# Kernel tuning notes

Hardware: AMD Instinct MI355X
Metric: run time of the kernel (lower is better)

Reference implementation:

```python
import jax, jax.numpy as jnp
import numpy as np

B, N, FIN = 4, 4096, 128
H, U = 4, 32

def setup_inputs() -> dict:
    key = jax.random.key(0)
    k = jax.random.split(key, 6)
    x = jax.random.normal(k[0], (B, N, FIN), dtype=jnp.float32)
    adj = (jax.random.uniform(k[1], (B, N, N)) < 0.05).astype(jnp.float32)
    glorot = lambda kk, shape, fi, fo: jax.random.uniform(kk, shape, jnp.float32,
                                                          -np.sqrt(6.0/(fi+fo)), np.sqrt(6.0/(fi+fo)))
    W = glorot(k[2], (FIN, H*U), FIN, H*U)
    a_src = glorot(k[3], (H, U, 1), U, 1)
    a_dst = glorot(k[4], (H, U, 1), U, 1)
    bias = jnp.zeros((H*U,), dtype=jnp.float32)
    return {"x": x, "adj": adj, "W": W, "a_src": a_src, "a_dst": a_dst, "bias": bias}

def reference(x, adj, W, a_src, a_dst, bias):
    # inference mode: attention dropout is a no-op
    b, n, _ = x.shape
    h_heads, u = a_src.shape[0], a_src.shape[1]
    # add self-loops, clip to {0,1}
    adj = jnp.clip(adj + jnp.eye(n, dtype=adj.dtype)[None], 0.0, 1.0)
    h = (x @ W).reshape(b, n, h_heads, u).transpose(0, 2, 1, 3)      # [B,H,N,U]
    f1 = jnp.einsum('bhnu,hu->bhn', h, a_src[..., 0])                # [B,H,N]
    f2 = jnp.einsum('bhnu,hu->bhn', h, a_dst[..., 0])                # [B,H,N]
    e = f1[:, :, :, None] + f2[:, :, None, :]                        # [B,H,N,N]
    e = jnp.where(e > 0, e, 0.2 * e)                                 # LeakyReLU(0.2)
    e = jnp.where(adj[:, None] > 0.0, e, jnp.float32(-1e9))
    alpha = jax.nn.softmax(e, axis=-1)
    out = jnp.einsum('bhij,bhju->bhiu', alpha, h)                    # [B,H,N,U]
    out = out.transpose(0, 2, 1, 3).reshape(b, n, h_heads * u) + bias
    return jnp.where(out > 0, out, jnp.expm1(out))                   # ELU
```

## Files before the change

kernel.cpp:

```cpp
#include <hip/hip_runtime.h>
#include <math.h>

#define NB   4
#define NN   4096
#define FIN  128
#define FOUT 128
#define NH   4
#define UU   32

#define K1_ROWS 64
#define K1_RT   8
#define K1_CT   4
#define XPAD    132

__global__ __launch_bounds__(256) void k1_feat(
    const float* __restrict__ x, const float* __restrict__ W,
    const float* __restrict__ a_src, const float* __restrict__ a_dst,
    float* __restrict__ hfeat, float* __restrict__ f1g, float* __restrict__ f2g)
{
    __shared__ __align__(16) float Wq[32 * FOUT];
    __shared__ __align__(16) float xs[K1_ROWS * XPAD];

    const int tid  = threadIdx.x;
    const int row0 = blockIdx.x * K1_ROWS;

    const float4* x4 = (const float4*)(x + (size_t)row0 * FIN);
    for (int idx = tid; idx < K1_ROWS * FIN / 4; idx += 256) {
        int r = idx >> 5, q = idx & 31;
        *(float4*)(xs + r * XPAD + q * 4) = x4[idx];
    }

    const int cg = tid & 31;
    const int rg = tid >> 5;
    float acc[K1_RT][K1_CT];
    #pragma unroll
    for (int rr = 0; rr < K1_RT; rr++)
        #pragma unroll
        for (int cc = 0; cc < K1_CT; cc++) acc[rr][cc] = 0.f;

    for (int kt = 0; kt < 4; kt++) {
        __syncthreads();
        for (int idx = tid; idx < 32 * FOUT / 4; idx += 256)
            ((float4*)Wq)[idx] = ((const float4*)W)[kt * 1024 + idx];
        __syncthreads();
        #pragma unroll
        for (int k4 = 0; k4 < 8; k4++) {
            const int kb = kt * 32 + k4 * 4;
            float4 xv[K1_RT];
            #pragma unroll
            for (int rr = 0; rr < K1_RT; rr++)
                xv[rr] = *(const float4*)(xs + (rg * K1_RT + rr) * XPAD + kb);
            #pragma unroll
            for (int kk = 0; kk < 4; kk++) {
                float wv[K1_CT];
                #pragma unroll
                for (int cc = 0; cc < K1_CT; cc++)
                    wv[cc] = Wq[(k4 * 4 + kk) * FOUT + cg + 32 * cc];
                #pragma unroll
                for (int rr = 0; rr < K1_RT; rr++) {
                    float xk = ((const float*)&xv[rr])[kk];
                    #pragma unroll
                    for (int cc = 0; cc < K1_CT; cc++)
                        acc[rr][cc] = fmaf(xk, wv[cc], acc[rr][cc]);
                }
            }
        }
    }
    __syncthreads();
    #pragma unroll
    for (int rr = 0; rr < K1_RT; rr++)
        #pragma unroll
        for (int cc = 0; cc < K1_CT; cc++)
            xs[(rg * K1_RT + rr) * XPAD + cg + 32 * cc] = acc[rr][cc];
    __syncthreads();

    float4* h4 = (float4*)(hfeat + (size_t)row0 * FOUT);
    for (int idx = tid; idx < K1_ROWS * FOUT / 4; idx += 256) {
        int r = idx >> 5, q = idx & 31;
        h4[idx] = *(const float4*)(xs + r * XPAD + q * 4);
    }

    for (int task = tid; task < K1_ROWS * NH * 2; task += 256) {
        int row = task >> 3;
        int head = (task >> 1) & 3;
        int which = task & 1;
        const float* av = which ? a_dst : a_src;
        float s = 0.f;
        #pragma unroll
        for (int u = 0; u < UU; u++)
            s += xs[row * XPAD + head * UU + u] * av[head * UU + u];
        float* dst = which ? f2g : f1g;
        dst[(size_t)(row0 + row) * NH + head] = s;
    }
}

#define CAP  512
#define APAD 516
#define PPAD 132

__global__ __launch_bounds__(256) void k2_gat(
    const float* __restrict__ adj, const float* __restrict__ hfeat,
    const float* __restrict__ f1g, const float* __restrict__ f2g,
    const float* __restrict__ bias, float* __restrict__ out)
{
    const int row  = blockIdx.x;
    const int b    = row >> 12;
    const int i    = row & (NN - 1);
    const int tid  = threadIdx.x;
    const int lane = tid & 63;
    const int wv   = tid >> 6;

    __shared__ int   nbr[CAP];
    __shared__ float alpha[NH][APAD];
    __shared__ float part[8][PPAD];
    __shared__ float inv_s[NH];
    __shared__ int   cnt_s;

    if (tid == 0) cnt_s = 0;
    __syncthreads();

    const float4* arow = (const float4*)(adj + (size_t)row * NN);
    float4 v[4];
    #pragma unroll
    for (int it = 0; it < 4; it++)
        v[it] = arow[wv * 256 + it * 64 + lane];

    const unsigned long long below = (1ull << lane) - 1ull;
    #pragma unroll
    for (int it = 0; it < 4; it++) {
        const int jb = (wv * 256 + it * 64 + lane) << 2;
        const bool p0 = (v[it].x > 0.f) | (jb + 0 == i);
        const bool p1 = (v[it].y > 0.f) | (jb + 1 == i);
        const bool p2 = (v[it].z > 0.f) | (jb + 2 == i);
        const bool p3 = (v[it].w > 0.f) | (jb + 3 == i);
        unsigned long long m0 = __ballot(p0), m1 = __ballot(p1);
        unsigned long long m2 = __ballot(p2), m3 = __ballot(p3);
        int c0 = __popcll(m0), c1 = __popcll(m1), c2 = __popcll(m2), c3 = __popcll(m3);
        int base = 0;
        if (lane == 0) base = atomicAdd(&cnt_s, c0 + c1 + c2 + c3);
        base = __shfl(base, 0, 64);
        if (p0) { int p = base + __popcll(m0 & below);                if (p < CAP) nbr[p] = jb + 0; }
        if (p1) { int p = base + c0 + __popcll(m1 & below);           if (p < CAP) nbr[p] = jb + 1; }
        if (p2) { int p = base + c0 + c1 + __popcll(m2 & below);      if (p < CAP) nbr[p] = jb + 2; }
        if (p3) { int p = base + c0 + c1 + c2 + __popcll(m3 & below); if (p < CAP) nbr[p] = jb + 3; }
    }
    __syncthreads();
    const int K = (cnt_s < CAP) ? cnt_s : CAP;

    const float4 f1v = ((const float4*)f1g)[row];
    for (int k = tid; k < K; k += 256) {
        int j = nbr[k];
        float4 f2v = ((const float4*)f2g)[(size_t)b * NN + j];
        float e0 = f1v.x + f2v.x; e0 = e0 > 0.f ? e0 : 0.2f * e0;
        float e1 = f1v.y + f2v.y; e1 = e1 > 0.f ? e1 : 0.2f * e1;
        float e2 = f1v.z + f2v.z; e2 = e2 > 0.f ? e2 : 0.2f * e2;
        float e3 = f1v.w + f2v.w; e3 = e3 > 0.f ? e3 : 0.2f * e3;
        alpha[0][k] = e0; alpha[1][k] = e1; alpha[2][k] = e2; alpha[3][k] = e3;
    }
    __syncthreads();

    {
        float m = -1e30f;
        for (int k = lane; k < K; k += 64) m = fmaxf(m, alpha[wv][k]);
        #pragma unroll
        for (int off = 32; off > 0; off >>= 1) m = fmaxf(m, __shfl_xor(m, off, 64));
        float s = 0.f;
        for (int k = lane; k < K; k += 64) {
            float a = __expf(alpha[wv][k] - m);
            alpha[wv][k] = a;
            s += a;
        }
        #pragma unroll
        for (int off = 32; off > 0; off >>= 1) s += __shfl_xor(s, off, 64);
        if (lane == 0) inv_s[wv] = 1.f / s;
    }
    __syncthreads();

    const int cq = tid & 31;
    const int kg = tid >> 5;
    const int hh = cq >> 3;
    const float* hb = hfeat + (size_t)b * NN * FOUT + cq * 4;
    float4 acc = make_float4(0.f, 0.f, 0.f, 0.f);
    int k = kg;
    for (; k + 8 < K; k += 16) {
        int j0 = nbr[k], j1 = nbr[k + 8];
        float a0 = alpha[hh][k], a1 = alpha[hh][k + 8];
        float4 h0 = *(const float4*)(hb + (size_t)j0 * FOUT);
        float4 h1 = *(const float4*)(hb + (size_t)j1 * FOUT);
        acc.x = fmaf(a0, h0.x, acc.x); acc.y = fmaf(a0, h0.y, acc.y);
        acc.z = fmaf(a0, h0.z, acc.z); acc.w = fmaf(a0, h0.w, acc.w);
        acc.x = fmaf(a1, h1.x, acc.x); acc.y = fmaf(a1, h1.y, acc.y);
        acc.z = fmaf(a1, h1.z, acc.z); acc.w = fmaf(a1, h1.w, acc.w);
    }
    if (k < K) {
        int j0 = nbr[k];
        float a0 = alpha[hh][k];
        float4 h0 = *(const float4*)(hb + (size_t)j0 * FOUT);
        acc.x = fmaf(a0, h0.x, acc.x); acc.y = fmaf(a0, h0.y, acc.y);
        acc.z = fmaf(a0, h0.z, acc.z); acc.w = fmaf(a0, h0.w, acc.w);
    }
    *(float4*)&part[kg][cq * 4] = acc;
    __syncthreads();

    if (tid < FOUT) {
        float o = 0.f;
        #pragma unroll
        for (int g = 0; g < 8; g++) o += part[g][tid];
        o = o * inv_s[tid >> 5] + bias[tid];
        o = o > 0.f ? o : expm1f(o);
        out[(size_t)row * FOUT + tid] = o;
    }
}

extern "C" void kernel_launch(void* const* d_in, const int* in_sizes, int n_in,
                              void* d_out, int out_size, void* d_ws, size_t ws_size,
                              hipStream_t stream) {
    const float* x     = (const float*)d_in[0];
    const float* adj   = (const float*)d_in[1];
    const float* W     = (const float*)d_in[2];
    const float* a_src = (const float*)d_in[3];
    const float* a_dst = (const float*)d_in[4];
    const float* bias  = (const float*)d_in[5];
    float* out = (float*)d_out;

    char* ws = (char*)d_ws;
    float* hfeat = (float*)ws;
    float* f1g   = (float*)(ws + (size_t)NB * NN * FOUT * 4);
    float* f2g   = f1g + (size_t)NB * NN * NH;

    k1_feat<<<NB * NN / K1_ROWS, 256, 0, stream>>>(x, W, a_src, a_dst, hfeat, f1g, f2g);
    k2_gat<<<NB * NN, 256, 0, stream>>>(adj, hfeat, f1g, f2g, bias, out);
}
```

Before: 420.7 us.

## Store features in bf16, fuse logit computation into compaction, remap blocks per XCD

Kernel 1 writes projected features as bf16, halving the bytes gathered per neighbor in the aggregation kernel. The neighbor compaction now uses a two-pass per-wave count and prefix instead of a shared atomic, and computes the LeakyReLU logits inline while writing neighbor indices. Block indices are remapped so each XCD processes a single batch, improving L2 reuse of the gathered features. This trades fp32 precision of h for bandwidth and adds a duplicate ballot pass over the adjacency row.

```diff
diff --git a/kernel.cpp b/kernel.cpp
--- a/kernel.cpp
+++ b/kernel.cpp
@@ -8,6 +8,12 @@
 #define NH   4
 #define UU   32
 
+__device__ __forceinline__ unsigned short f2bf(float f) {
+    unsigned u = __float_as_uint(f);
+    u += 0x7fff + ((u >> 16) & 1);
+    return (unsigned short)(u >> 16);
+}
+
 #define K1_ROWS 64
 #define K1_RT   8
 #define K1_CT   4
@@ -16,7 +22,7 @@
 __global__ __launch_bounds__(256) void k1_feat(
     const float* __restrict__ x, const float* __restrict__ W,
     const float* __restrict__ a_src, const float* __restrict__ a_dst,
-    float* __restrict__ hfeat, float* __restrict__ f1g, float* __restrict__ f2g)
+    unsigned short* __restrict__ hbf, float* __restrict__ f1g, float* __restrict__ f2g)
 {
     __shared__ __align__(16) float Wq[32 * FOUT];
     __shared__ __align__(16) float xs[K1_ROWS * XPAD];
@@ -74,10 +80,16 @@
             xs[(rg * K1_RT + rr) * XPAD + cg + 32 * cc] = acc[rr][cc];
     __syncthreads();
 
-    float4* h4 = (float4*)(hfeat + (size_t)row0 * FOUT);
-    for (int idx = tid; idx < K1_ROWS * FOUT / 4; idx += 256) {
-        int r = idx >> 5, q = idx & 31;
-        h4[idx] = *(const float4*)(xs + r * XPAD + q * 4);
+    unsigned short* hrow = hbf + (size_t)row0 * FOUT;
+    for (int idx = tid; idx < K1_ROWS * FOUT / 8; idx += 256) {
+        int r = idx >> 4, q = idx & 15;
+        const float* src = xs + r * XPAD + q * 8;
+        uint4 o;
+        o.x = (unsigned)f2bf(src[0]) | ((unsigned)f2bf(src[1]) << 16);
+        o.y = (unsigned)f2bf(src[2]) | ((unsigned)f2bf(src[3]) << 16);
+        o.z = (unsigned)f2bf(src[4]) | ((unsigned)f2bf(src[5]) << 16);
+        o.w = (unsigned)f2bf(src[6]) | ((unsigned)f2bf(src[7]) << 16);
+        *(uint4*)(hrow + (size_t)r * FOUT + q * 8) = o;
     }
 
     for (int task = tid; task < K1_ROWS * NH * 2; task += 256) {
@@ -94,30 +106,31 @@
     }
 }
 
-#define CAP  512
-#define APAD 516
-#define PPAD 132
+#define CAP   512
+#define APAD  516
+#define PPART 132
+
+__device__ __forceinline__ float lrelu(float e) { return e > 0.f ? e : 0.2f * e; }
 
 __global__ __launch_bounds__(256) void k2_gat(
-    const float* __restrict__ adj, const float* __restrict__ hfeat,
+    const float* __restrict__ adj, const unsigned short* __restrict__ hbf,
     const float* __restrict__ f1g, const float* __restrict__ f2g,
     const float* __restrict__ bias, float* __restrict__ out)
 {
-    const int row  = blockIdx.x;
-    const int b    = row >> 12;
-    const int i    = row & (NN - 1);
+    const int q    = blockIdx.x;
+    const int xcd  = q & 7;
+    const int b    = xcd >> 1;
+    const int i    = ((q >> 3) << 1) | (xcd & 1);
+    const int row  = b * NN + i;
     const int tid  = threadIdx.x;
     const int lane = tid & 63;
     const int wv   = tid >> 6;
 
     __shared__ int   nbr[CAP];
     __shared__ float alpha[NH][APAD];
-    __shared__ float part[8][PPAD];
+    __shared__ float part[16][PPART];
     __shared__ float inv_s[NH];
-    __shared__ int   cnt_s;
-
-    if (tid == 0) cnt_s = 0;
-    __syncthreads();
+    __shared__ int   wcnt[4];
 
     const float4* arow = (const float4*)(adj + (size_t)row * NN);
     float4 v[4];
@@ -126,6 +139,25 @@
         v[it] = arow[wv * 256 + it * 64 + lane];
 
     const unsigned long long below = (1ull << lane) - 1ull;
+    int my_cnt = 0;
+    #pragma unroll
+    for (int it = 0; it < 4; it++) {
+        const int jb = (wv * 256 + it * 64 + lane) << 2;
+        my_cnt += __popcll(__ballot((v[it].x > 0.f) | (jb + 0 == i)));
+        my_cnt += __popcll(__ballot((v[it].y > 0.f) | (jb + 1 == i)));
+        my_cnt += __popcll(__ballot((v[it].z > 0.f) | (jb + 2 == i)));
+        my_cnt += __popcll(__ballot((v[it].w > 0.f) | (jb + 3 == i)));
+    }
+    if (lane == 0) wcnt[wv] = my_cnt;
+    __syncthreads();
+
+    const int w0 = wcnt[0], w1 = wcnt[1], w2 = wcnt[2], w3 = wcnt[3];
+    int run = (wv > 0 ? w0 : 0) + (wv > 1 ? w1 : 0) + (wv > 2 ? w2 : 0);
+    const int total = w0 + w1 + w2 + w3;
+    const int K = (total < CAP) ? total : CAP;
+
+    const float4* f2b = (const float4*)(f2g + (size_t)b * NN * NH);
+    const float4  f1v = ((const float4*)f1g)[row];
     #pragma unroll
     for (int it = 0; it < 4; it++) {
         const int jb = (wv * 256 + it * 64 + lane) << 2;
@@ -136,26 +168,25 @@
         unsigned long long m0 = __ballot(p0), m1 = __ballot(p1);
         unsigned long long m2 = __ballot(p2), m3 = __ballot(p3);
         int c0 = __popcll(m0), c1 = __popcll(m1), c2 = __popcll(m2), c3 = __popcll(m3);
-        int base = 0;
-        if (lane == 0) base = atomicAdd(&cnt_s, c0 + c1 + c2 + c3);
-        base = __shfl(base, 0, 64);
-        if (p0) { int p = base + __popcll(m0 & below);                if (p < CAP) nbr[p] = jb + 0; }
-        if (p1) { int p = base + c0 + __popcll(m1 & below);           if (p < CAP) nbr[p] = jb + 1; }
-        if (p2) { int p = base + c0 + c1 + __popcll(m2 & below);      if (p < CAP) nbr[p] = jb + 2; }
-        if (p3) { int p = base + c0 + c1 + c2 + __popcll(m3 & below); if (p < CAP) nbr[p] = jb + 3; }
-    }
-    __syncthreads();
-    const int K = (cnt_s < CAP) ? cnt_s : CAP;
-
-    const float4 f1v = ((const float4*)f1g)[row];
-    for (int k = tid; k < K; k += 256) {
-        int j = nbr[k];
-        float4 f2v = ((const float4*)f2g)[(size_t)b * NN + j];
-        float e0 = f1v.x + f2v.x; e0 = e0 > 0.f ? e0 : 0.2f * e0;
-        float e1 = f1v.y + f2v.y; e1 = e1 > 0.f ? e1 : 0.2f * e1;
-        float e2 = f1v.z + f2v.z; e2 = e2 > 0.f ? e2 : 0.2f * e2;
-        float e3 = f1v.w + f2v.w; e3 = e3 > 0.f ? e3 : 0.2f * e3;
-        alpha[0][k] = e0; alpha[1][k] = e1; alpha[2][k] = e2; alpha[3][k] = e3;
+        #pragma unroll
+        for (int e = 0; e < 4; e++) {
+            bool pe = e == 0 ? p0 : e == 1 ? p1 : e == 2 ? p2 : p3;
+            unsigned long long me = e == 0 ? m0 : e == 1 ? m1 : e == 2 ? m2 : m3;
+            int pre = e == 0 ? 0 : e == 1 ? c0 : e == 2 ? c0 + c1 : c0 + c1 + c2;
+            if (pe) {
+                int p = run + pre + __popcll(me & below);
+                if (p < CAP) {
+                    int j = jb + e;
+                    nbr[p] = j;
+                    float4 f2v = f2b[j];
+                    alpha[0][p] = lrelu(f1v.x + f2v.x);
+                    alpha[1][p] = lrelu(f1v.y + f2v.y);
+                    alpha[2][p] = lrelu(f1v.z + f2v.z);
+                    alpha[3][p] = lrelu(f1v.w + f2v.w);
+                }
+            }
+        }
+        run += c0 + c1 + c2 + c3;
     }
     __syncthreads();
 
@@ -176,36 +207,52 @@
     }
     __syncthreads();
 
-    const int cq = tid & 31;
-    const int kg = tid >> 5;
-    const int hh = cq >> 3;
-    const float* hb = hfeat + (size_t)b * NN * FOUT + cq * 4;
-    float4 acc = make_float4(0.f, 0.f, 0.f, 0.f);
+    const int cq = tid & 15;
+    const int kg = tid >> 4;
+    const int hh = cq >> 2;
+    const unsigned short* hb = hbf + (size_t)b * NN * FOUT + cq * 8;
+    float acc[8];
+    #pragma unroll
+    for (int t = 0; t < 8; t++) acc[t] = 0.f;
+
     int k = kg;
-    for (; k + 8 < K; k += 16) {
-        int j0 = nbr[k], j1 = nbr[k + 8];
-        float a0 = alpha[hh][k], a1 = alpha[hh][k + 8];
-        float4 h0 = *(const float4*)(hb + (size_t)j0 * FOUT);
-        float4 h1 = *(const float4*)(hb + (size_t)j1 * FOUT);
-        acc.x = fmaf(a0, h0.x, acc.x); acc.y = fmaf(a0, h0.y, acc.y);
-        acc.z = fmaf(a0, h0.z, acc.z); acc.w = fmaf(a0, h0.w, acc.w);
-        acc.x = fmaf(a1, h1.x, acc.x); acc.y = fmaf(a1, h1.y, acc.y);
-        acc.z = fmaf(a1, h1.z, acc.z); acc.w = fmaf(a1, h1.w, acc.w);
+    for (; k + 16 < K; k += 32) {
+        int j0 = nbr[k], j1 = nbr[k + 16];
+        float a0 = alpha[hh][k], a1 = alpha[hh][k + 16];
+        uint4 u4a = *(const uint4*)(hb + (size_t)j0 * FOUT);
+        uint4 u4b = *(const uint4*)(hb + (size_t)j1 * FOUT);
+        const unsigned* u0 = (const unsigned*)&u4a;
+        const unsigned* u1 = (const unsigned*)&u4b;
+        #pragma unroll
+        for (int t = 0; t < 4; t++) {
+            acc[2*t]   = fmaf(a0, __uint_as_float(u0[t] << 16),          acc[2*t]);
+            acc[2*t+1] = fmaf(a0, __uint_as_float(u0[t] & 0xffff0000u),  acc[2*t+1]);
+        }
+        #pragma unroll
+        for (int t = 0; t < 4; t++) {
+            acc[2*t]   = fmaf(a1, __uint_as_float(u1[t] << 16),          acc[2*t]);
+            acc[2*t+1] = fmaf(a1, __uint_as_float(u1[t] & 0xffff0000u),  acc[2*t+1]);
+        }
     }
     if (k < K) {
         int j0 = nbr[k];
         float a0 = alpha[hh][k];
-        float4 h0 = *(const float4*)(hb + (size_t)j0 * FOUT);
-        acc.x = fmaf(a0, h0.x, acc.x); acc.y = fmaf(a0, h0.y, acc.y);
-        acc.z = fmaf(a0, h0.z, acc.z); acc.w = fmaf(a0, h0.w, acc.w);
-    }
-    *(float4*)&part[kg][cq * 4] = acc;
+        uint4 u4a = *(const uint4*)(hb + (size_t)j0 * FOUT);
+        const unsigned* u0 = (const unsigned*)&u4a;
+        #pragma unroll
+        for (int t = 0; t < 4; t++) {
+            acc[2*t]   = fmaf(a0, __uint_as_float(u0[t] << 16),          acc[2*t]);
+            acc[2*t+1] = fmaf(a0, __uint_as_float(u0[t] & 0xffff0000u),  acc[2*t+1]);
+        }
+    }
+    *(float4*)&part[kg][cq * 8]     = *(float4*)&acc[0];
+    *(float4*)&part[kg][cq * 8 + 4] = *(float4*)&acc[4];
     __syncthreads();
 
     if (tid < FOUT) {
         float o = 0.f;
         #pragma unroll
-        for (int g = 0; g < 8; g++) o += part[g][tid];
+        for (int g = 0; g < 16; g++) o += part[g][tid];
         o = o * inv_s[tid >> 5] + bias[tid];
         o = o > 0.f ? o : expm1f(o);
         out[(size_t)row * FOUT + tid] = o;
@@ -224,10 +271,10 @@
     float* out = (float*)d_out;
 
     char* ws = (char*)d_ws;
-    float* hfeat = (float*)ws;
-    float* f1g   = (float*)(ws + (size_t)NB * NN * FOUT * 4);
-    float* f2g   = f1g + (size_t)NB * NN * NH;
-
-    k1_feat<<<NB * NN / K1_ROWS, 256, 0, stream>>>(x, W, a_src, a_dst, hfeat, f1g, f2g);
-    k2_gat<<<NB * NN, 256, 0, stream>>>(adj, hfeat, f1g, f2g, bias, out);
-}
+    unsigned short* hbf = (unsigned short*)ws;
+    float* f1g = (float*)(ws + (size_t)NB * NN * FOUT * 2);
+    float* f2g = f1g + (size_t)NB * NN * NH;
+
+    k1_feat<<<NB * NN / K1_ROWS, 256, 0, stream>>>(x, W, a_src, a_dst, hbf, f1g, f2g);
+    k2_gat<<<NB * NN, 256, 0, stream>>>(adj, hbf, f1g, f2g, bias, out);
+}
```

After: 427.6 us. About the same (+1.7%).
